# Kernel optimization log

Hardware: AMD Instinct MI355X
Metric: run time of the kernel (lower is better)

## Reference

```python
import jax, jax.numpy as jnp
import numpy as np

DIM = 768
NUM_HEADS = 12
HEAD_DIM = DIM // NUM_HEADS
SCALE = HEAD_DIM ** -0.5


def setup_inputs() -> dict:
    key = jax.random.key(0)
    k_x, k_qkv, k_proj, k_pb = jax.random.split(key, 4)
    B, N = 16, 1024
    x = jax.random.normal(k_x, (B, N, DIM), dtype=jnp.float32)
    # nn.Linear weights: stored as [out, in]; qkv_bias=False -> no qkv bias
    w_qkv = jax.random.normal(k_qkv, (3 * DIM, DIM), dtype=jnp.float32) * (DIM ** -0.5)
    w_proj = jax.random.normal(k_proj, (DIM, DIM), dtype=jnp.float32) * (DIM ** -0.5)
    b_proj = jax.random.normal(k_pb, (DIM,), dtype=jnp.float32) * 0.01
    return {"x": x, "w_qkv": w_qkv, "w_proj": w_proj, "b_proj": b_proj}


def reference(x, w_qkv, w_proj, b_proj):
    B, N, C = x.shape
    H, D = NUM_HEADS, HEAD_DIM
    # qkv projection: [B,N,3C] -> [3,B,H,N,D]
    qkv = jnp.einsum('bnc,oc->bno', x, w_qkv)
    qkv = qkv.reshape(B, N, 3, H, D).transpose(2, 0, 3, 1, 4)
    q, k, v = qkv[0], qkv[1], qkv[2]
    # scaled dot-product attention (dropout ratios are 0.0 -> identity)
    attn = jnp.einsum('bhnd,bhmd->bhnm', q, k) * SCALE
    attn = jax.nn.softmax(attn, axis=-1)
    out = jnp.einsum('bhnm,bhmd->bhnd', attn, v)
    out = out.transpose(0, 2, 1, 3).reshape(B, N, C)
    # output projection
    return jnp.einsum('bnc,oc->bno', out, w_proj) + b_proj
```

## Files before the change

### kernel.cpp

```cpp
#include <hip/hip_runtime.h>
#include <hip/hip_bf16.h>
#include <stdint.h>

typedef unsigned short u16;
typedef unsigned int   u32;
typedef short bf16x8 __attribute__((ext_vector_type(8)));
typedef float f32x4  __attribute__((ext_vector_type(4)));
typedef float f32x16 __attribute__((ext_vector_type(16)));

#define MFMA16(A,B,C) __builtin_amdgcn_mfma_f32_16x16x32_bf16((A),(B),(C),0,0,0)
#define MFMA32(A,B,C) __builtin_amdgcn_mfma_f32_32x32x16_bf16((A),(B),(C),0,0,0)

__device__ __forceinline__ u16 f2b(float x) {
  u32 u = __float_as_uint(x);
  u += 0x7fffu + ((u >> 16) & 1u);
  return (u16)(u >> 16);
}
__device__ __forceinline__ u32 cvtpk(float lo, float hi) {
  u32 r;
  asm("v_cvt_pk_bf16_f32 %0, %1, %2" : "=v"(r) : "v"(lo), "v"(hi));
  return r;
}

typedef __attribute__((address_space(1))) const void glob_void;
typedef __attribute__((address_space(3))) void lds_void;
__device__ __forceinline__ void gld16(const void* g, void* s) {
  __builtin_amdgcn_global_load_lds((glob_void*)g, (lds_void*)s, 16, 0, 0);
}

__global__ void cvt_bf16(const float4* __restrict__ in, ushort4* __restrict__ out, int n4) {
  int stride = gridDim.x * blockDim.x;
  for (int i = blockIdx.x * blockDim.x + threadIdx.x; i < n4; i += stride) {
    float4 v = in[i];
    ushort4 o;
    o.x = f2b(v.x); o.y = f2b(v.y); o.z = f2b(v.z); o.w = f2b(v.w);
    out[i] = o;
  }
}

__global__ __launch_bounds__(256) void gemm_qkv(
    const u16* __restrict__ xb, const u16* __restrict__ wb,
    u16* __restrict__ q, u16* __restrict__ k, u16* __restrict__ vt)
{
  __shared__ u16 lA[2][128*32];
  __shared__ u16 lB[2][128*32];
  const int tid = threadIdx.x;
  const int lane = tid & 63;
  const int wv = tid >> 6;
  const int wr = wv >> 1, wc = wv & 1;
  const int m0 = blockIdx.x << 7;
  const int o0 = blockIdx.y << 7;
  f32x4 acc[4][4] = {};
  const int srow = tid >> 2;
  const int sb   = (((tid & 3) ^ ((srow >> 1) & 3)) << 4);
  const char* gA0 = (const char*)(xb + (size_t)(m0 + srow)      * 768) + sb;
  const char* gA1 = (const char*)(xb + (size_t)(m0 + 64 + srow) * 768) + sb;
  const char* gB0 = (const char*)(wb + (size_t)(o0 + srow)      * 768) + sb;
  const char* gB1 = (const char*)(wb + (size_t)(o0 + 64 + srow) * 768) + sb;
  char* sA = (char*)lA + tid * 16;
  char* sB = (char*)lB + tid * 16;
  const int frow = lane & 15;
  const int fk   = (((lane >> 4) ^ ((frow >> 1) & 3)) << 4);

#define QKV_STAGE(buf, kt) do { const int kb_ = (kt) << 6; const int bo_ = (buf) << 13; \
    gld16(gA0 + kb_, sA + bo_); gld16(gA1 + kb_, sA + bo_ + 4096); \
    gld16(gB0 + kb_, sB + bo_); gld16(gB1 + kb_, sB + bo_ + 4096); } while (0)

  QKV_STAGE(0, 0);
  asm volatile("s_waitcnt vmcnt(0) lgkmcnt(0)" ::: "memory");
  __builtin_amdgcn_s_barrier();
  for (int kt = 0; kt < 24; ++kt) {
    const int cur = kt & 1;
    if (kt < 23) QKV_STAGE(cur ^ 1, kt + 1);
    const char* bA = (const char*)lA + (cur << 13);
    const char* bB = (const char*)lB + (cur << 13);
    bf16x8 af[4], bfr[4];
#pragma unroll
    for (int m = 0; m < 4; ++m)
      af[m] = *(const bf16x8*)(bA + ((wr*64 + m*16 + frow) << 6) + fk);
#pragma unroll
    for (int n = 0; n < 4; ++n)
      bfr[n] = *(const bf16x8*)(bB + ((wc*64 + n*16 + frow) << 6) + fk);
#pragma unroll
    for (int m = 0; m < 4; ++m)
#pragma unroll
      for (int n = 0; n < 4; ++n)
        acc[m][n] = MFMA16(af[m], bfr[n], acc[m][n]);
    asm volatile("s_waitcnt vmcnt(0) lgkmcnt(0)" ::: "memory");
    __builtin_amdgcn_s_barrier();
  }
  const int which = o0 / 768;
  const int ob = o0 - which * 768;
  const float QSCALE = 0.18033688011112042f;
#pragma unroll
  for (int n = 0; n < 4; ++n) {
    const int go = ob + wc*64 + n*16 + (lane & 15);
    const int h = go >> 6, d = go & 63;
#pragma unroll
    for (int m = 0; m < 4; ++m) {
      const int gm0 = m0 + wr*64 + m*16 + ((lane >> 4) << 2);
      const int b = gm0 >> 10, nn0 = gm0 & 1023;
      if (which == 2) {
        ushort4 o4;
        o4.x = f2b(acc[m][n][0]); o4.y = f2b(acc[m][n][1]);
        o4.z = f2b(acc[m][n][2]); o4.w = f2b(acc[m][n][3]);
        *(ushort4*)(vt + (((size_t)((b*12 + h)*64 + d)) << 10) + nn0) = o4;
      } else if (which == 0) {
#pragma unroll
        for (int r = 0; r < 4; ++r)
          q[((size_t)((b*12 + h)*1024 + nn0 + r) << 6) + d] = f2b(acc[m][n][r] * QSCALE);
      } else {
#pragma unroll
        for (int r = 0; r < 4; ++r)
          k[((size_t)((b*12 + h)*1024 + nn0 + r) << 6) + d] = f2b(acc[m][n][r]);
      }
    }
  }
}

__global__ __launch_bounds__(512) void attn_fwd(
    const u16* __restrict__ q, const u16* __restrict__ kk,
    const u16* __restrict__ vt, u16* __restrict__ ao)
{
  __shared__ u16 lK[2][64*64];
  __shared__ u16 lV[2][64*64];
  const int tid = threadIdx.x, lane = tid & 63, wv = tid >> 6;
  const int l31 = lane & 31, hh = lane >> 5;
  const int bh = blockIdx.x, qt = blockIdx.y;
  const u16*  qb = q  + ((size_t)bh << 16);
  const char* kg = (const char*)(kk + ((size_t)bh << 16));
  const char* vg = (const char*)(vt + ((size_t)bh << 16));
  const int qrow = (qt << 8) + (wv << 5) + l31;
  bf16x8 qreg[4];
#pragma unroll
  for (int c = 0; c < 4; ++c)
    qreg[c] = *(const bf16x8*)((const char*)qb + (size_t)qrow*128 + c*32 + hh*16);
  f32x16 ot[2] = {};
  float mrun = -1e30f, lrun = 0.f;
  const int o1 = tid << 4;
  const int ko1 = o1 ^ (((o1 >> 7) & 7) << 4);
  const int d1 = o1 >> 7;
  const int vo1 = d1*2048 + ((o1 & 127) ^ ((d1 & 7) << 4));
  char* sK = (char*)lK;
  char* sV = (char*)lV;

#define ATTN_STAGE(buf, t) do { const int bo_ = (buf) << 13; \
    gld16(kg + ((t) << 13) + ko1, sK + bo_ + o1); \
    gld16(vg + ((t) << 7) + vo1, sV + bo_ + o1); } while (0)

  ATTN_STAGE(0, 0);
  asm volatile("s_waitcnt vmcnt(0) lgkmcnt(0)" ::: "memory");
  __builtin_amdgcn_s_barrier();
  for (int t0 = 0; t0 < 16; ++t0) {
    const int cur = t0 & 1;
    if (t0 < 15) ATTN_STAGE(cur ^ 1, t0 + 1);
    const char* bK = (const char*)lK + (cur << 13);
    const char* bV = (const char*)lV + (cur << 13);
    f32x16 s[2] = {};
#pragma unroll
    for (int tt = 0; tt < 2; ++tt) {
      const int row = (tt << 5) + l31;
      const int rb = row << 7;
      const int sw = (row & 7) << 4;
#pragma unroll
      for (int c = 0; c < 4; ++c) {
        bf16x8 kf = *(const bf16x8*)(bK + rb + (((c << 5) + (hh << 4)) ^ sw));
        s[tt] = MFMA32(kf, qreg[c], s[tt]);
      }
    }
    float mloc = s[0][0];
#pragma unroll
    for (int tt = 0; tt < 2; ++tt)
#pragma unroll
      for (int r = 0; r < 16; ++r) mloc = fmaxf(mloc, s[tt][r]);
    if (!__all(mloc <= mrun + 8.f)) {
      mloc = fmaxf(mloc, __shfl_xor(mloc, 32));
      const float mnew  = fmaxf(mrun, mloc);
      const float alpha = __builtin_amdgcn_exp2f(mrun - mnew);
      lrun *= alpha;
#pragma unroll
      for (int dt = 0; dt < 2; ++dt)
#pragma unroll
        for (int r = 0; r < 16; ++r) ot[dt][r] *= alpha;
      mrun = mnew;
    }
    float sum = 0.f;
#pragma unroll
    for (int tt = 0; tt < 2; ++tt)
#pragma unroll
      for (int r = 0; r < 16; ++r) {
        s[tt][r] = __builtin_amdgcn_exp2f(s[tt][r] - mrun);
        sum += s[tt][r];
      }
    sum += __shfl_xor(sum, 32);
    lrun += sum;
    bf16x8 pb[4];
#pragma unroll
    for (int tt = 0; tt < 2; ++tt) {
      u32 x0 = cvtpk(s[tt][0],  s[tt][1]);
      u32 y0 = cvtpk(s[tt][4],  s[tt][5]);
      u32 x1 = cvtpk(s[tt][2],  s[tt][3]);
      u32 y1 = cvtpk(s[tt][6],  s[tt][7]);
      asm("v_permlane32_swap_b32 %0, %1" : "+v"(x0), "+v"(y0));
      asm("v_permlane32_swap_b32 %0, %1" : "+v"(x1), "+v"(y1));
      u32 x2 = cvtpk(s[tt][8],  s[tt][9]);
      u32 y2 = cvtpk(s[tt][12], s[tt][13]);
      u32 x3 = cvtpk(s[tt][10], s[tt][11]);
      u32 y3 = cvtpk(s[tt][14], s[tt][15]);
      asm("v_permlane32_swap_b32 %0, %1" : "+v"(x2), "+v"(y2));
      asm("v_permlane32_swap_b32 %0, %1" : "+v"(x3), "+v"(y3));
      union { u32 u[4]; bf16x8 v; } a, b;
      a.u[0] = x0; a.u[1] = x1; a.u[2] = y0; a.u[3] = y1;
      b.u[0] = x2; b.u[1] = x3; b.u[2] = y2; b.u[3] = y3;
      pb[2*tt]     = a.v;
      pb[2*tt + 1] = b.v;
    }
#pragma unroll
    for (int dt = 0; dt < 2; ++dt) {
      const int row = (dt << 5) + l31;
      const int rb = row << 7;
      const int sw = (row & 7) << 4;
#pragma unroll
      for (int cc = 0; cc < 4; ++cc) {
        bf16x8 vf = *(const bf16x8*)(bV + rb + (((cc << 5) + (hh << 4)) ^ sw));
        ot[dt] = MFMA32(vf, pb[cc], ot[dt]);
      }
    }
    asm volatile("s_waitcnt vmcnt(0) lgkmcnt(0)" ::: "memory");
    __builtin_amdgcn_s_barrier();
  }
  const float linv = 1.f / lrun;
  const int b = bh / 12, h = bh - b * 12;
  u16* po = ao + ((size_t)(b*1024 + qrow)) * 768 + h*64;
#pragma unroll
  for (int dt = 0; dt < 2; ++dt) {
#pragma unroll
    for (int g = 0; g < 4; ++g) {
      ushort4 o4;
      o4.x = f2b(ot[dt][4*g + 0] * linv);
      o4.y = f2b(ot[dt][4*g + 1] * linv);
      o4.z = f2b(ot[dt][4*g + 2] * linv);
      o4.w = f2b(ot[dt][4*g + 3] * linv);
      *(ushort4*)(po + dt*32 + g*8 + hh*4) = o4;
    }
  }
}

__global__ __launch_bounds__(256) void gemm_proj(
    const u16* __restrict__ ab, const u16* __restrict__ wb,
    const float* __restrict__ bias, float* __restrict__ out)
{
  __shared__ u16 lA[2][128*32];
  __shared__ u16 lB[2][128*32];
  const int tid = threadIdx.x;
  const int lane = tid & 63;
  const int wv = tid >> 6;
  const int wr = wv >> 1, wc = wv & 1;
  const int m0 = blockIdx.x << 7;
  const int o0 = blockIdx.y << 7;
  f32x4 acc[4][4] = {};
  const int srow = tid >> 2;
  const int sb   = (((tid & 3) ^ ((srow >> 1) & 3)) << 4);
  const char* gA0 = (const char*)(ab + (size_t)(m0 + srow)      * 768) + sb;
  const char* gA1 = (const char*)(ab + (size_t)(m0 + 64 + srow) * 768) + sb;
  const char* gB0 = (const char*)(wb + (size_t)(o0 + srow)      * 768) + sb;
  const char* gB1 = (const char*)(wb + (size_t)(o0 + 64 + srow) * 768) + sb;
  char* sA = (char*)lA + tid * 16;
  char* sB = (char*)lB + tid * 16;
  const int frow = lane & 15;
  const int fk   = (((lane >> 4) ^ ((frow >> 1) & 3)) << 4);

  QKV_STAGE(0, 0);
  asm volatile("s_waitcnt vmcnt(0) lgkmcnt(0)" ::: "memory");
  __builtin_amdgcn_s_barrier();
  for (int kt = 0; kt < 24; ++kt) {
    const int cur = kt & 1;
    if (kt < 23) QKV_STAGE(cur ^ 1, kt + 1);
    const char* bA = (const char*)lA + (cur << 13);
    const char* bB = (const char*)lB + (cur << 13);
    bf16x8 af[4], bfr[4];
#pragma unroll
    for (int m = 0; m < 4; ++m)
      af[m] = *(const bf16x8*)(bA + ((wr*64 + m*16 + frow) << 6) + fk);
#pragma unroll
    for (int n = 0; n < 4; ++n)
      bfr[n] = *(const bf16x8*)(bB + ((wc*64 + n*16 + frow) << 6) + fk);
#pragma unroll
    for (int m = 0; m < 4; ++m)
#pragma unroll
      for (int n = 0; n < 4; ++n)
        acc[m][n] = MFMA16(af[m], bfr[n], acc[m][n]);
    asm volatile("s_waitcnt vmcnt(0) lgkmcnt(0)" ::: "memory");
    __builtin_amdgcn_s_barrier();
  }
#pragma unroll
  for (int n = 0; n < 4; ++n) {
    const int go = o0 + wc*64 + n*16 + (lane & 15);
    const float bv = bias[go];
#pragma unroll
    for (int m = 0; m < 4; ++m) {
#pragma unroll
      for (int r = 0; r < 4; ++r) {
        const int gm = m0 + wr*64 + m*16 + ((lane >> 4) << 2) + r;
        out[(size_t)gm * 768 + go] = acc[m][n][r] + bv;
      }
    }
  }
}

extern "C" void kernel_launch(void* const* d_in, const int* in_sizes, int n_in,
                              void* d_out, int out_size, void* d_ws, size_t ws_size,
                              hipStream_t stream)
{
  (void)in_sizes; (void)n_in; (void)out_size; (void)ws_size;
  const float* x  = (const float*)d_in[0];
  const float* wq = (const float*)d_in[1];
  const float* wp = (const float*)d_in[2];
  const float* bp = (const float*)d_in[3];
  float* out = (float*)d_out;
  char* ws = (char*)d_ws;
  u16* xb     = (u16*)(ws);
  u16* wqkvb  = (u16*)(ws + 25165824);
  u16* wprojb = (u16*)(ws + 28704768);
  u16* qa     = (u16*)(ws + 29884416);
  u16* ka     = (u16*)(ws + 55050240);
  u16* vta    = (u16*)(ws + 80216064);
  u16* ao     = xb;

  cvt_bf16<<<2048, 256, 0, stream>>>((const float4*)x,  (ushort4*)xb,     3145728);
  cvt_bf16<<<1024, 256, 0, stream>>>((const float4*)wq, (ushort4*)wqkvb,   442368);
  cvt_bf16<<< 576, 256, 0, stream>>>((const float4*)wp, (ushort4*)wprojb,  147456);
  gemm_qkv<<<dim3(128, 18), 256, 0, stream>>>(xb, wqkvb, qa, ka, vta);
  attn_fwd<<<dim3(192, 4), 512, 0, stream>>>(qa, ka, vta, ao);
  gemm_proj<<<dim3(128, 6), 256, 0, stream>>>(ao, wprojb, bp, out);
}
```

Baseline: 205.2 us.

## Deepen LDS pipelines to four buffers and enlarge QKV GEMM tiles

All three main kernels move from double-buffered LDS staging with a full vmcnt(0) wait plus barrier at the end of each iteration to a 4-slot ring that keeps two stages in flight. Each iteration now uses a partial vmcnt wait and a single barrier. The QKV GEMM also grows from 128x128 tiles on 256 threads to 256x256 tiles on 512 threads, with 8x4 accumulators per wave, raising operand reuse. The GEMMs additionally raise wave priority around the MFMA block. In exchange, LDS use and register pressure go up (128KB LDS for qkv), and the larger tiles leave a smaller grid (576 blocks), which may reduce occupancy.

```diff
diff --git a/kernel.cpp b/kernel.cpp
--- a/kernel.cpp
+++ b/kernel.cpp
@@ -38,67 +38,68 @@
   }
 }
 
-__global__ __launch_bounds__(256) void gemm_qkv(
+__global__ __launch_bounds__(512) void gemm_qkv(
     const u16* __restrict__ xb, const u16* __restrict__ wb,
     u16* __restrict__ q, u16* __restrict__ k, u16* __restrict__ vt)
 {
-  __shared__ u16 lA[2][128*32];
-  __shared__ u16 lB[2][128*32];
+  __shared__ u16 lA[4][256*32];
+  __shared__ u16 lB[4][256*32];
   const int tid = threadIdx.x;
   const int lane = tid & 63;
   const int wv = tid >> 6;
-  const int wr = wv >> 1, wc = wv & 1;
-  const int m0 = blockIdx.x << 7;
-  const int o0 = blockIdx.y << 7;
-  f32x4 acc[4][4] = {};
+  const int wr = wv >> 2, wc = wv & 3;
+  const int m0 = blockIdx.x << 8;
+  const int by = blockIdx.y;
+  const int o0 = by << 8;
+  f32x4 acc[8][4] = {};
   const int srow = tid >> 2;
   const int sb   = (((tid & 3) ^ ((srow >> 1) & 3)) << 4);
-  const char* gA0 = (const char*)(xb + (size_t)(m0 + srow)      * 768) + sb;
-  const char* gA1 = (const char*)(xb + (size_t)(m0 + 64 + srow) * 768) + sb;
-  const char* gB0 = (const char*)(wb + (size_t)(o0 + srow)      * 768) + sb;
-  const char* gB1 = (const char*)(wb + (size_t)(o0 + 64 + srow) * 768) + sb;
+  const char* gA0 = (const char*)(xb + (size_t)(m0 + srow) * 768) + sb;
+  const char* gB0 = (const char*)(wb + (size_t)(o0 + srow) * 768) + sb;
   char* sA = (char*)lA + tid * 16;
   char* sB = (char*)lB + tid * 16;
   const int frow = lane & 15;
   const int fk   = (((lane >> 4) ^ ((frow >> 1) & 3)) << 4);
 
-#define QKV_STAGE(buf, kt) do { const int kb_ = (kt) << 6; const int bo_ = (buf) << 13; \
-    gld16(gA0 + kb_, sA + bo_); gld16(gA1 + kb_, sA + bo_ + 4096); \
-    gld16(gB0 + kb_, sB + bo_); gld16(gB1 + kb_, sB + bo_ + 4096); } while (0)
-
-  QKV_STAGE(0, 0);
-  asm volatile("s_waitcnt vmcnt(0) lgkmcnt(0)" ::: "memory");
-  __builtin_amdgcn_s_barrier();
-  for (int kt = 0; kt < 24; ++kt) {
-    const int cur = kt & 1;
-    if (kt < 23) QKV_STAGE(cur ^ 1, kt + 1);
-    const char* bA = (const char*)lA + (cur << 13);
-    const char* bB = (const char*)lB + (cur << 13);
-    bf16x8 af[4], bfr[4];
-#pragma unroll
-    for (int m = 0; m < 4; ++m)
-      af[m] = *(const bf16x8*)(bA + ((wr*64 + m*16 + frow) << 6) + fk);
+#define QSTG(t) do { const int kb_ = (t) << 6; const int bo_ = ((t) & 3) << 14; \
+    gld16(gA0 + kb_,          sA + bo_); \
+    gld16(gA0 + kb_ + 196608, sA + bo_ + 8192); \
+    gld16(gB0 + kb_,          sB + bo_); \
+    gld16(gB0 + kb_ + 196608, sB + bo_ + 8192); } while (0)
+
+  QSTG(0);
+  QSTG(1);
+  for (int t = 0; t < 24; ++t) {
+    if (t < 23) asm volatile("s_waitcnt vmcnt(4)" ::: "memory");
+    else        asm volatile("s_waitcnt vmcnt(0)" ::: "memory");
+    __builtin_amdgcn_s_barrier();
+    if (t < 22) QSTG(t + 2);
+    const char* bA = (const char*)lA + ((t & 3) << 14);
+    const char* bB = (const char*)lB + ((t & 3) << 14);
+    bf16x8 bfr[4];
 #pragma unroll
     for (int n = 0; n < 4; ++n)
       bfr[n] = *(const bf16x8*)(bB + ((wc*64 + n*16 + frow) << 6) + fk);
-#pragma unroll
-    for (int m = 0; m < 4; ++m)
+    __builtin_amdgcn_s_setprio(1);
+#pragma unroll
+    for (int m = 0; m < 8; ++m) {
+      bf16x8 af = *(const bf16x8*)(bA + ((wr*128 + m*16 + frow) << 6) + fk);
 #pragma unroll
       for (int n = 0; n < 4; ++n)
-        acc[m][n] = MFMA16(af[m], bfr[n], acc[m][n]);
-    asm volatile("s_waitcnt vmcnt(0) lgkmcnt(0)" ::: "memory");
-    __builtin_amdgcn_s_barrier();
-  }
-  const int which = o0 / 768;
-  const int ob = o0 - which * 768;
+        acc[m][n] = MFMA16(af, bfr[n], acc[m][n]);
+    }
+    __builtin_amdgcn_s_setprio(0);
+  }
+  const int which = by / 3;
+  const int ob = (by - which * 3) << 8;
   const float QSCALE = 0.18033688011112042f;
 #pragma unroll
   for (int n = 0; n < 4; ++n) {
-    const int go = ob + wc*64 + n*16 + (lane & 15);
+    const int go = ob + wc*64 + n*16 + frow;
     const int h = go >> 6, d = go & 63;
 #pragma unroll
-    for (int m = 0; m < 4; ++m) {
-      const int gm0 = m0 + wr*64 + m*16 + ((lane >> 4) << 2);
+    for (int m = 0; m < 8; ++m) {
+      const int gm0 = m0 + wr*128 + m*16 + ((lane >> 4) << 2);
       const int b = gm0 >> 10, nn0 = gm0 & 1023;
       if (which == 2) {
         ushort4 o4;
@@ -122,8 +123,8 @@
     const u16* __restrict__ q, const u16* __restrict__ kk,
     const u16* __restrict__ vt, u16* __restrict__ ao)
 {
-  __shared__ u16 lK[2][64*64];
-  __shared__ u16 lV[2][64*64];
+  __shared__ u16 lK[4][64*64];
+  __shared__ u16 lV[4][64*64];
   const int tid = threadIdx.x, lane = tid & 63, wv = tid >> 6;
   const int l31 = lane & 31, hh = lane >> 5;
   const int bh = blockIdx.x, qt = blockIdx.y;
@@ -144,18 +145,19 @@
   char* sK = (char*)lK;
   char* sV = (char*)lV;
 
-#define ATTN_STAGE(buf, t) do { const int bo_ = (buf) << 13; \
+#define ATTN_STAGE(t) do { const int bo_ = ((t) & 3) << 13; \
     gld16(kg + ((t) << 13) + ko1, sK + bo_ + o1); \
     gld16(vg + ((t) << 7) + vo1, sV + bo_ + o1); } while (0)
 
-  ATTN_STAGE(0, 0);
-  asm volatile("s_waitcnt vmcnt(0) lgkmcnt(0)" ::: "memory");
-  __builtin_amdgcn_s_barrier();
+  ATTN_STAGE(0);
+  ATTN_STAGE(1);
   for (int t0 = 0; t0 < 16; ++t0) {
-    const int cur = t0 & 1;
-    if (t0 < 15) ATTN_STAGE(cur ^ 1, t0 + 1);
-    const char* bK = (const char*)lK + (cur << 13);
-    const char* bV = (const char*)lV + (cur << 13);
+    if (t0 < 15) asm volatile("s_waitcnt vmcnt(2)" ::: "memory");
+    else         asm volatile("s_waitcnt vmcnt(0)" ::: "memory");
+    __builtin_amdgcn_s_barrier();
+    if (t0 < 14) ATTN_STAGE(t0 + 2);
+    const char* bK = (const char*)lK + ((t0 & 3) << 13);
+    const char* bV = (const char*)lV + ((t0 & 3) << 13);
     f32x16 s[2] = {};
 #pragma unroll
     for (int tt = 0; tt < 2; ++tt) {
@@ -226,8 +228,6 @@
         ot[dt] = MFMA32(vf, pb[cc], ot[dt]);
       }
     }
-    asm volatile("s_waitcnt vmcnt(0) lgkmcnt(0)" ::: "memory");
-    __builtin_amdgcn_s_barrier();
   }
   const float linv = 1.f / lrun;
   const int b = bh / 12, h = bh - b * 12;
@@ -250,8 +250,8 @@
     const u16* __restrict__ ab, const u16* __restrict__ wb,
     const float* __restrict__ bias, float* __restrict__ out)
 {
-  __shared__ u16 lA[2][128*32];
-  __shared__ u16 lB[2][128*32];
+  __shared__ u16 lA[4][128*32];
+  __shared__ u16 lB[4][128*32];
   const int tid = threadIdx.x;
   const int lane = tid & 63;
   const int wv = tid >> 6;
@@ -270,14 +270,19 @@
   const int frow = lane & 15;
   const int fk   = (((lane >> 4) ^ ((frow >> 1) & 3)) << 4);
 
-  QKV_STAGE(0, 0);
-  asm volatile("s_waitcnt vmcnt(0) lgkmcnt(0)" ::: "memory");
-  __builtin_amdgcn_s_barrier();
-  for (int kt = 0; kt < 24; ++kt) {
-    const int cur = kt & 1;
-    if (kt < 23) QKV_STAGE(cur ^ 1, kt + 1);
-    const char* bA = (const char*)lA + (cur << 13);
-    const char* bB = (const char*)lB + (cur << 13);
+#define PSTG(t) do { const int kb_ = (t) << 6; const int bo_ = ((t) & 3) << 13; \
+    gld16(gA0 + kb_, sA + bo_); gld16(gA1 + kb_, sA + bo_ + 4096); \
+    gld16(gB0 + kb_, sB + bo_); gld16(gB1 + kb_, sB + bo_ + 4096); } while (0)
+
+  PSTG(0);
+  PSTG(1);
+  for (int t = 0; t < 24; ++t) {
+    if (t < 23) asm volatile("s_waitcnt vmcnt(4)" ::: "memory");
+    else        asm volatile("s_waitcnt vmcnt(0)" ::: "memory");
+    __builtin_amdgcn_s_barrier();
+    if (t < 22) PSTG(t + 2);
+    const char* bA = (const char*)lA + ((t & 3) << 13);
+    const char* bB = (const char*)lB + ((t & 3) << 13);
     bf16x8 af[4], bfr[4];
 #pragma unroll
     for (int m = 0; m < 4; ++m)
@@ -285,13 +290,13 @@
 #pragma unroll
     for (int n = 0; n < 4; ++n)
       bfr[n] = *(const bf16x8*)(bB + ((wc*64 + n*16 + frow) << 6) + fk);
+    __builtin_amdgcn_s_setprio(1);
 #pragma unroll
     for (int m = 0; m < 4; ++m)
 #pragma unroll
       for (int n = 0; n < 4; ++n)
         acc[m][n] = MFMA16(af[m], bfr[n], acc[m][n]);
-    asm volatile("s_waitcnt vmcnt(0) lgkmcnt(0)" ::: "memory");
-    __builtin_amdgcn_s_barrier();
+    __builtin_amdgcn_s_setprio(0);
   }
 #pragma unroll
   for (int n = 0; n < 4; ++n) {
@@ -330,7 +335,7 @@
   cvt_bf16<<<2048, 256, 0, stream>>>((const float4*)x,  (ushort4*)xb,     3145728);
   cvt_bf16<<<1024, 256, 0, stream>>>((const float4*)wq, (ushort4*)wqkvb,   442368);
   cvt_bf16<<< 576, 256, 0, stream>>>((const float4*)wp, (ushort4*)wprojb,  147456);
-  gemm_qkv<<<dim3(128, 18), 256, 0, stream>>>(xb, wqkvb, qa, ka, vta);
+  gemm_qkv<<<dim3(64, 9), 512, 0, stream>>>(xb, wqkvb, qa, ka, vta);
   attn_fwd<<<dim3(192, 4), 512, 0, stream>>>(qa, ka, vta, ao);
   gemm_proj<<<dim3(128, 6), 256, 0, stream>>>(ao, wprojb, bp, out);
 }
```

New measurement: 245.7 us. 19.7% more time.

## Retile QKV GEMM to 256x256 blocks with phased staging and priority hints

Applied to the files above, without the earlier changes.

The QKV projection GEMM moves from 128x128 tiles with 256 threads to 256x256 tiles with 512 threads (8 waves) and a 64-wide K step. Loads are split into four phases interleaved with MFMA groups, using partial vmcnt waits, an XOR swizzle, and s_setprio around the MFMA bursts. The aim is more operand reuse per LDS byte, fewer global loads, and better overlap of loads with compute. The cost is 128KB of LDS and more accumulator registers, which may reduce occupancy, and the grid drops to 576 blocks.

```diff
diff --git a/kernel.cpp b/kernel.cpp
--- a/kernel.cpp
+++ b/kernel.cpp
@@ -38,67 +38,86 @@
   }
 }
 
-__global__ __launch_bounds__(256) void gemm_qkv(
+__global__ __launch_bounds__(512) void gemm_qkv(
     const u16* __restrict__ xb, const u16* __restrict__ wb,
     u16* __restrict__ q, u16* __restrict__ k, u16* __restrict__ vt)
 {
-  __shared__ u16 lA[2][128*32];
-  __shared__ u16 lB[2][128*32];
+  __shared__ u16 lA[2][256*64];
+  __shared__ u16 lB[2][256*64];
   const int tid = threadIdx.x;
   const int lane = tid & 63;
   const int wv = tid >> 6;
-  const int wr = wv >> 1, wc = wv & 1;
-  const int m0 = blockIdx.x << 7;
-  const int o0 = blockIdx.y << 7;
-  f32x4 acc[4][4] = {};
-  const int srow = tid >> 2;
-  const int sb   = (((tid & 3) ^ ((srow >> 1) & 3)) << 4);
-  const char* gA0 = (const char*)(xb + (size_t)(m0 + srow)      * 768) + sb;
-  const char* gA1 = (const char*)(xb + (size_t)(m0 + 64 + srow) * 768) + sb;
-  const char* gB0 = (const char*)(wb + (size_t)(o0 + srow)      * 768) + sb;
-  const char* gB1 = (const char*)(wb + (size_t)(o0 + 64 + srow) * 768) + sb;
+  const int wr = wv >> 2, wc = wv & 3;
+  const int m0 = blockIdx.x << 8;
+  const int by = blockIdx.y;
+  const int o0 = by << 8;
+  f32x4 acc[8][4] = {};
+  const int srow = tid >> 3;
+  const int sg   = (((tid & 7) ^ (srow & 7)) << 4);
+  const char* gA = (const char*)xb + (size_t)(m0 + srow) * 1536 + sg;
+  const char* gB = (const char*)wb + (size_t)(o0 + srow) * 1536 + sg;
   char* sA = (char*)lA + tid * 16;
   char* sB = (char*)lB + tid * 16;
-  const int frow = lane & 15;
-  const int fk   = (((lane >> 4) ^ ((frow >> 1) & 3)) << 4);
-
-#define QKV_STAGE(buf, kt) do { const int kb_ = (kt) << 6; const int bo_ = (buf) << 13; \
-    gld16(gA0 + kb_, sA + bo_); gld16(gA1 + kb_, sA + bo_ + 4096); \
-    gld16(gB0 + kb_, sB + bo_); gld16(gB1 + kb_, sB + bo_ + 4096); } while (0)
-
-  QKV_STAGE(0, 0);
-  asm volatile("s_waitcnt vmcnt(0) lgkmcnt(0)" ::: "memory");
-  __builtin_amdgcn_s_barrier();
-  for (int kt = 0; kt < 24; ++kt) {
-    const int cur = kt & 1;
-    if (kt < 23) QKV_STAGE(cur ^ 1, kt + 1);
-    const char* bA = (const char*)lA + (cur << 13);
-    const char* bB = (const char*)lB + (cur << 13);
-    bf16x8 af[4], bfr[4];
-#pragma unroll
-    for (int m = 0; m < 4; ++m)
-      af[m] = *(const bf16x8*)(bA + ((wr*64 + m*16 + frow) << 6) + fk);
-#pragma unroll
-    for (int n = 0; n < 4; ++n)
-      bfr[n] = *(const bf16x8*)(bB + ((wc*64 + n*16 + frow) << 6) + fk);
-#pragma unroll
-    for (int m = 0; m < 4; ++m)
-#pragma unroll
-      for (int n = 0; n < 4; ++n)
-        acc[m][n] = MFMA16(af[m], bfr[n], acc[m][n]);
-    asm volatile("s_waitcnt vmcnt(0) lgkmcnt(0)" ::: "memory");
-    __builtin_amdgcn_s_barrier();
-  }
-  const int which = o0 / 768;
-  const int ob = o0 - which * 768;
+  const int frow = lane & 15, hh = lane >> 4;
+  const int swz = (frow & 7) << 4;
+  const int fc0 = ((hh << 4)      ) ^ swz;
+  const int fc1 = ((hh << 4) + 64 ) ^ swz;
+
+#define STGA(t1, c) gld16(gA + (size_t)(c)*98304 + (size_t)(t1)*128, \
+                          sA + (((t1) & 1) << 15) + ((c) << 13))
+#define STGB(t1, c) gld16(gB + (size_t)(c)*98304 + (size_t)(t1)*128, \
+                          sB + (((t1) & 1) << 15) + ((c) << 13))
+
+#define QPHASE(MH, FC, STG_PAIR) do { \
+    bf16x8 af_[4], bf_[4]; \
+    _Pragma("unroll") \
+    for (int i_ = 0; i_ < 4; ++i_) \
+      af_[i_] = *(const bf16x8*)(bA + ((wr*128 + (MH)*64 + i_*16 + frow) << 7) + (FC)); \
+    _Pragma("unroll") \
+    for (int n_ = 0; n_ < 4; ++n_) \
+      bf_[n_] = *(const bf16x8*)(bB + ((wc*64 + n_*16 + frow) << 7) + (FC)); \
+    if (st) { STG_PAIR; } \
+    __builtin_amdgcn_s_barrier(); \
+    __builtin_amdgcn_s_setprio(1); \
+    _Pragma("unroll") \
+    for (int i_ = 0; i_ < 4; ++i_) \
+      _Pragma("unroll") \
+      for (int n_ = 0; n_ < 4; ++n_) \
+        acc[(MH)*4 + i_][n_] = MFMA16(af_[i_], bf_[n_], acc[(MH)*4 + i_][n_]); \
+    __builtin_amdgcn_s_setprio(0); \
+  } while (0)
+
+  STGB(0, 0); STGB(0, 1); STGB(0, 2); STGB(0, 3);
+  STGA(0, 0); STGA(0, 2); STGA(0, 1); STGA(0, 3);
+
+  for (int t = 0; t < 12; ++t) {
+    const char* bA = (const char*)lA + ((t & 1) << 15);
+    const char* bB = (const char*)lB + ((t & 1) << 15);
+    const bool st = (t < 11);
+    const int tn = t + 1;
+    asm volatile("s_waitcnt vmcnt(2)" ::: "memory");
+    __builtin_amdgcn_s_barrier();
+    QPHASE(0, fc0, STGB(tn, 0); STGB(tn, 1));
+    __builtin_amdgcn_s_barrier();
+    QPHASE(0, fc1, STGB(tn, 2); STGB(tn, 3));
+    if (st) asm volatile("s_waitcnt vmcnt(4)" ::: "memory");
+    else    asm volatile("s_waitcnt vmcnt(0)" ::: "memory");
+    __builtin_amdgcn_s_barrier();
+    QPHASE(1, fc0, STGA(tn, 0); STGA(tn, 2));
+    __builtin_amdgcn_s_barrier();
+    QPHASE(1, fc1, STGA(tn, 1); STGA(tn, 3));
+  }
+
+  const int which = by / 3;
+  const int ob = (by - which * 3) << 8;
   const float QSCALE = 0.18033688011112042f;
 #pragma unroll
   for (int n = 0; n < 4; ++n) {
-    const int go = ob + wc*64 + n*16 + (lane & 15);
+    const int go = ob + wc*64 + n*16 + frow;
     const int h = go >> 6, d = go & 63;
 #pragma unroll
-    for (int m = 0; m < 4; ++m) {
-      const int gm0 = m0 + wr*64 + m*16 + ((lane >> 4) << 2);
+    for (int m = 0; m < 8; ++m) {
+      const int gm0 = m0 + wr*128 + m*16 + ((lane >> 4) << 2);
       const int b = gm0 >> 10, nn0 = gm0 & 1023;
       if (which == 2) {
         ushort4 o4;
@@ -250,8 +269,8 @@
     const u16* __restrict__ ab, const u16* __restrict__ wb,
     const float* __restrict__ bias, float* __restrict__ out)
 {
-  __shared__ u16 lA[2][128*32];
-  __shared__ u16 lB[2][128*32];
+  __shared__ u16 lAp[2][128*32];
+  __shared__ u16 lBp[2][128*32];
   const int tid = threadIdx.x;
   const int lane = tid & 63;
   const int wv = tid >> 6;
@@ -265,19 +284,23 @@
   const char* gA1 = (const char*)(ab + (size_t)(m0 + 64 + srow) * 768) + sb;
   const char* gB0 = (const char*)(wb + (size_t)(o0 + srow)      * 768) + sb;
   const char* gB1 = (const char*)(wb + (size_t)(o0 + 64 + srow) * 768) + sb;
-  char* sA = (char*)lA + tid * 16;
-  char* sB = (char*)lB + tid * 16;
+  char* sAp = (char*)lAp + tid * 16;
+  char* sBp = (char*)lBp + tid * 16;
   const int frow = lane & 15;
   const int fk   = (((lane >> 4) ^ ((frow >> 1) & 3)) << 4);
 
-  QKV_STAGE(0, 0);
+#define PSTG(buf, kt) do { const int kb_ = (kt) << 6; const int bo_ = (buf) << 13; \
+    gld16(gA0 + kb_, sAp + bo_); gld16(gA1 + kb_, sAp + bo_ + 4096); \
+    gld16(gB0 + kb_, sBp + bo_); gld16(gB1 + kb_, sBp + bo_ + 4096); } while (0)
+
+  PSTG(0, 0);
   asm volatile("s_waitcnt vmcnt(0) lgkmcnt(0)" ::: "memory");
   __builtin_amdgcn_s_barrier();
   for (int kt = 0; kt < 24; ++kt) {
     const int cur = kt & 1;
-    if (kt < 23) QKV_STAGE(cur ^ 1, kt + 1);
-    const char* bA = (const char*)lA + (cur << 13);
-    const char* bB = (const char*)lB + (cur << 13);
+    if (kt < 23) PSTG(cur ^ 1, kt + 1);
+    const char* bA = (const char*)lAp + (cur << 13);
+    const char* bB = (const char*)lBp + (cur << 13);
     bf16x8 af[4], bfr[4];
 #pragma unroll
     for (int m = 0; m < 4; ++m)
@@ -330,7 +353,7 @@
   cvt_bf16<<<2048, 256, 0, stream>>>((const float4*)x,  (ushort4*)xb,     3145728);
   cvt_bf16<<<1024, 256, 0, stream>>>((const float4*)wq, (ushort4*)wqkvb,   442368);
   cvt_bf16<<< 576, 256, 0, stream>>>((const float4*)wp, (ushort4*)wprojb,  147456);
-  gemm_qkv<<<dim3(128, 18), 256, 0, stream>>>(xb, wqkvb, qa, ka, vta);
+  gemm_qkv<<<dim3(64, 9), 512, 0, stream>>>(xb, wqkvb, qa, ka, vta);
   attn_fwd<<<dim3(192, 4), 512, 0, stream>>>(qa, ka, vta, ao);
   gemm_proj<<<dim3(128, 6), 256, 0, stream>>>(ao, wprojb, bp, out);
 }
```

After: 208.8 us. Within noise of the previous version (+1.7%).
